# Performance work log

Hardware: AMD Instinct MI355X
Metric: run time of the kernel (lower is better)

## Reference

```python
import jax, jax.numpy as jnp
import numpy as np


def setup_inputs() -> dict:
    key = jax.random.key(0)
    k1, k2, k3, k4 = jax.random.split(key, 4)
    S, D, DKQ, DV = 8192, 2048, 128, 128
    x = jax.random.normal(k1, (S, D), dtype=jnp.float32)
    w_q = jax.random.uniform(k2, (D, DKQ), dtype=jnp.float32)
    w_k = jax.random.uniform(k3, (D, DKQ), dtype=jnp.float32)
    w_v = jax.random.uniform(k4, (D, DV), dtype=jnp.float32)
    return {"x": x, "w_q": w_q, "w_k": w_k, "w_v": w_v}


def reference(x, w_q, w_k, w_v):
    # x: [S, D]; single-head causal attention, unbatched as in the source.
    dim_kq = w_q.shape[1]
    q = x @ w_q  # [S, DKQ]
    k = x @ w_k  # [S, DKQ]
    v = x @ w_v  # [S, DV]
    scores = (q @ k.T) / jnp.sqrt(jnp.asarray(dim_kq, q.dtype))  # [S, S]
    S = scores.shape[0]
    causal = jnp.tril(jnp.ones((S, S), dtype=bool))
    scores = jnp.where(causal, scores, -jnp.inf)
    att_w = jax.nn.softmax(scores, axis=-1)
    return att_w @ v  # [S, DV]
```

## Files before the change

### kernel.cpp

```cpp
#include <hip/hip_runtime.h>

#define S_LEN 8192
#define D_DIM 2048
#define HD    128
#define KVB   32
#define NCH   16
#define QTR   256

typedef __attribute__((ext_vector_type(8))) short bf16x8;
typedef __attribute__((ext_vector_type(4))) float f32x4;

__device__ __forceinline__ unsigned short f2bf(float f) {
  unsigned int u = __float_as_uint(f);
  u += 0x7fffu + ((u >> 16) & 1u);
  return (unsigned short)(u >> 16);
}
__device__ __forceinline__ float bf2f(unsigned short h) {
  return __uint_as_float(((unsigned int)h) << 16);
}

__device__ __forceinline__ void glds16(const void* g, const short* l) {
  __builtin_amdgcn_global_load_lds(
      (const __attribute__((address_space(1))) void*)g,
      (__attribute__((address_space(3))) void*)l, 16, 0, 0);
}

__global__ __launch_bounds__(256)
void split_w_kernel(const float* __restrict__ wq, const float* __restrict__ wk,
                    const float* __restrict__ wv,
                    unsigned short* __restrict__ wTh, unsigned short* __restrict__ wTl)
{
  const int mode = blockIdx.y;
  const float* __restrict__ w = (mode == 0) ? wq : (mode == 1) ? wk : wv;
  unsigned short* __restrict__ oh = wTh + (size_t)mode * HD * D_DIM;
  unsigned short* __restrict__ ol = wTl + (size_t)mode * HD * D_DIM;
  const int k0 = blockIdx.x * 64;

  __shared__ float ws[64][132];
  const int t = threadIdx.x;
#pragma unroll
  for (int i = 0; i < 8; ++i) {
    int idx = t + i * 256;
    int row = idx >> 5;
    int c4  = idx & 31;
    *(float4*)&ws[row][c4 * 4] = *(const float4*)(w + (size_t)(k0 + row) * HD + c4 * 4);
  }
  __syncthreads();
#pragma unroll
  for (int i = 0; i < 4; ++i) {
    int task = t + i * 256;
    int col = task >> 3;
    int kc  = task & 7;
    ushort4 h[2], l[2];
#pragma unroll
    for (int e = 0; e < 8; ++e) {
      float f = ws[kc * 8 + e][col];
      unsigned short hb = f2bf(f);
      ((unsigned short*)&h[e >> 2])[e & 3] = hb;
      ((unsigned short*)&l[e >> 2])[e & 3] = f2bf(f - bf2f(hb));
    }
    size_t off = (size_t)col * D_DIM + k0 + kc * 8;
    *(ushort4*)(oh + off)     = h[0];
    *(ushort4*)(oh + off + 4) = h[1];
    *(ushort4*)(ol + off)     = l[0];
    *(ushort4*)(ol + off + 4) = l[1];
  }
}

__global__ __launch_bounds__(256)
void proj_kernel(const float* __restrict__ x,
                 const unsigned short* __restrict__ wTh, const unsigned short* __restrict__ wTl,
                 unsigned short* __restrict__ q_hi, unsigned short* __restrict__ q_lo,
                 unsigned short* __restrict__ k_hi, unsigned short* __restrict__ k_lo,
                 unsigned short* __restrict__ vT)
{
  __shared__ short sm[2][12288];

  const int mode = blockIdx.y;
  const int mt   = blockIdx.x;
  const bool split = (mode < 2);

  const unsigned short* gwh = wTh + (size_t)mode * HD * D_DIM;
  const unsigned short* gwl = wTl + (size_t)mode * HD * D_DIM;

  const int t   = threadIdx.x;
  const int wid = t >> 6;
  const int ln  = t & 63;
  const int cl  = ln & 15;
  const int g4  = ln >> 4;

  const int slotx = wid * 64 + ln;
  const int rowx  = slotx >> 2, scx = slotx & 3;
  const int kofx  = (scx ^ (rowx & 3)) * 8;
  const float* gx = x + (size_t)(mt * 64 + rowx) * D_DIM + kofx;

  auto stagew = [&](int kt, int buf) {
    short* b = sm[buf];
#pragma unroll
    for (int g = 0; g < 2; ++g) {
      int slot = g * 256 + wid * 64 + ln;
      int col = slot >> 2, sc = slot & 3;
      int kof = (sc ^ (col & 3)) * 8;
      glds16(gwh + (size_t)col * D_DIM + kt + kof, b + 4096 + (g * 256 + wid * 64) * 8);
      if (split)
        glds16(gwl + (size_t)col * D_DIM + kt + kof, b + 8192 + (g * 256 + wid * 64) * 8);
    }
  };
  auto writex = [&](const float4& a0, const float4& a1, int buf) {
    short* b = sm[buf];
    float fv[8];
    *(float4*)&fv[0] = a0;
    *(float4*)&fv[4] = a1;
    bf16x8 hv, lv;
#pragma unroll
    for (int e = 0; e < 8; ++e) {
      unsigned short hb = f2bf(fv[e]);
      hv[e] = (short)hb;
      lv[e] = (short)f2bf(fv[e] - bf2f(hb));
    }
    *(bf16x8*)(b + slotx * 8) = hv;
    if (split) *(bf16x8*)(b + 2048 + slotx * 8) = lv;
  };

  f32x4 acc[2][4];
#pragma unroll
  for (int m = 0; m < 2; ++m)
#pragma unroll
    for (int n = 0; n < 4; ++n) acc[m][n] = f32x4{0.f, 0.f, 0.f, 0.f};

  {
    float4 a0 = *(const float4*)(gx + 0);
    float4 a1 = *(const float4*)(gx + 4);
    stagew(0, 0);
    writex(a0, a1, 0);
  }
  __syncthreads();

  for (int kt = 0, step = 0; kt < D_DIM; kt += 32, ++step) {
    const int cur = step & 1;
    const bool more = (kt + 32 < D_DIM);
    float4 n0, n1;
    if (more) {
      n0 = *(const float4*)(gx + kt + 32);
      n1 = *(const float4*)(gx + kt + 36);
      stagew(kt + 32, cur ^ 1);
    }

    const short* b = sm[cur];
    bf16x8 a_h[2], a_l[2], b_h[4], b_l[4];
#pragma unroll
    for (int m = 0; m < 2; ++m) {
      int row = (wid >> 1) * 32 + m * 16 + cl;
      int byte = row * 64 + ((g4 ^ (row & 3)) << 4);
      a_h[m] = *(const bf16x8*)((const char*)b + byte);
      if (split) a_l[m] = *(const bf16x8*)((const char*)b + 4096 + byte);
    }
#pragma unroll
    for (int n = 0; n < 4; ++n) {
      int col = (wid & 1) * 64 + n * 16 + cl;
      int byte = col * 64 + ((g4 ^ (col & 3)) << 4);
      b_h[n] = *(const bf16x8*)((const char*)b + 8192 + byte);
      if (split) b_l[n] = *(const bf16x8*)((const char*)b + 16384 + byte);
    }

#pragma unroll
    for (int m = 0; m < 2; ++m)
#pragma unroll
      for (int n = 0; n < 4; ++n)
        acc[m][n] = __builtin_amdgcn_mfma_f32_16x16x32_bf16(a_h[m], b_h[n], acc[m][n], 0, 0, 0);
    if (split) {
#pragma unroll
      for (int m = 0; m < 2; ++m)
#pragma unroll
        for (int n = 0; n < 4; ++n) {
          acc[m][n] = __builtin_amdgcn_mfma_f32_16x16x32_bf16(a_l[m], b_h[n], acc[m][n], 0, 0, 0);
          acc[m][n] = __builtin_amdgcn_mfma_f32_16x16x32_bf16(a_h[m], b_l[n], acc[m][n], 0, 0, 0);
        }
    }
    if (more) writex(n0, n1, cur ^ 1);
    __syncthreads();
  }

  const int rbase = mt * 64 + (wid >> 1) * 32 + g4 * 4;
  const int cbase = (wid & 1) * 64 + cl;

  if (mode < 2) {
    const float scale = (mode == 0) ? 0.08838834764831843f : 1.0f;
    unsigned short* __restrict__ oh = (mode == 0) ? q_hi : k_hi;
    unsigned short* __restrict__ ol = (mode == 0) ? q_lo : k_lo;
#pragma unroll
    for (int m = 0; m < 2; ++m)
#pragma unroll
      for (int n = 0; n < 4; ++n)
#pragma unroll
        for (int r = 0; r < 4; ++r) {
          float val = acc[m][n][r] * scale;
          unsigned short hb = f2bf(val);
          size_t off = (size_t)(rbase + m * 16 + r) * HD + cbase + n * 16;
          oh[off] = hb;
          ol[off] = f2bf(val - bf2f(hb));
        }
  } else {
#pragma unroll
    for (int m = 0; m < 2; ++m)
#pragma unroll
      for (int n = 0; n < 4; ++n) {
        ushort4 o;
#pragma unroll
        for (int r = 0; r < 4; ++r) ((unsigned short*)&o)[r] = f2bf(acc[m][n][r]);
        int col = cbase + n * 16;
        *(ushort4*)(vT + (size_t)col * S_LEN + rbase + m * 16) = o;
      }
  }
}

__global__ __launch_bounds__(512)
void attn_kernel(const unsigned short* __restrict__ q_hi, const unsigned short* __restrict__ q_lo,
                 const unsigned short* __restrict__ k_hi, const unsigned short* __restrict__ k_lo,
                 const unsigned short* __restrict__ vT,
                 unsigned short* __restrict__ part_o, float* __restrict__ part_ml)
{
  extern __shared__ short smem[];
  short* ls_kh = smem;
  short* ls_kl = ls_kh + 8192;
  short* ls_v  = ls_kl + 8192;
  short* ls_ql = ls_v + 8192;
  short* ls_p  = ls_ql + 32768;

  const int t   = threadIdx.x;
  const int wid = t >> 6;
  const int ln  = t & 63;
  const int cl  = ln & 15;
  const int g4  = ln >> 4;
  const int pairId = blockIdx.x >> 4;
  const int chunk  = blockIdx.x & 15;

  short* pw = ls_p + wid * 1280;

  auto stage = [&](int j, int buf) {
    const unsigned short* gkh = k_hi + (size_t)j * KVB * HD;
    const unsigned short* gkl = k_lo + (size_t)j * KVB * HD;
    const unsigned short* gv  = vT + (size_t)j * KVB;
    {
      int row = t >> 4, sc = t & 15;
      int c16 = sc ^ (row & 7);
      glds16(gkh + row * HD + c16 * 8, ls_kh + buf * 4096 + t * 8);
      glds16(gkl + row * HD + c16 * 8, ls_kl + buf * 4096 + t * 8);
    }
    {
      int d = t >> 2, sub = t & 3;
      int s2 = sub ^ ((d >> 1) & 3);
      glds16(gv + (size_t)d * S_LEN + s2 * 8, ls_v + buf * 4096 + t * 8);
    }
  };

  for (int hh = 0; hh < 2; ++hh) {
    const int T = hh ? (31 - pairId) : pairId;
    const int jmaxB = 8 * T + 7;
    const int jmaxW = 8 * T + wid;
    const int rowbase = T * QTR + wid * 32;

    {
      const unsigned short* gql = q_lo + (size_t)T * QTR * HD;
#pragma unroll
      for (int i = 0; i < 8; ++i) {
        int slot = i * 512 + t;
        int row = slot >> 4, sc = slot & 15;
        int c16 = sc ^ (row & 7);
        glds16(gql + (size_t)row * HD + c16 * 8, ls_ql + slot * 8);
      }
    }

    bf16x8 qh[2][4];
#pragma unroll
    for (int rg = 0; rg < 2; ++rg) {
      const size_t qoff = ((size_t)rowbase + rg * 16 + cl) * HD + g4 * 8;
#pragma unroll
      for (int kc = 0; kc < 4; ++kc)
        qh[rg][kc] = *(const bf16x8*)(q_hi + qoff + kc * 32);
    }

    float m_i[2][4], l_i[2][4];
    f32x4 o_acc[2][8];
#pragma unroll
    for (int rg = 0; rg < 2; ++rg)
#pragma unroll
      for (int i = 0; i < 4; ++i) { m_i[rg][i] = -1e30f; l_i[rg][i] = 0.f; }
#pragma unroll
    for (int rg = 0; rg < 2; ++rg)
#pragma unroll
      for (int c2 = 0; c2 < 8; ++c2) o_acc[rg][c2] = f32x4{0.f, 0.f, 0.f, 0.f};

    if (chunk <= jmaxB) {
      int cur = 0;
      stage(chunk, 0);
      __syncthreads();
      for (int j = chunk; j <= jmaxB; j += NCH) {
        if (j + NCH <= jmaxB) stage(j + NCH, cur ^ 1);

        if (j <= jmaxW) {
          const int rl0 = wid * 32 + cl;
          const int rl1 = rl0 + 16;
          f32x4 s[2][2];
          s[0][0] = f32x4{0.f, 0.f, 0.f, 0.f};
          s[0][1] = f32x4{0.f, 0.f, 0.f, 0.f};
          s[1][0] = f32x4{0.f, 0.f, 0.f, 0.f};
          s[1][1] = f32x4{0.f, 0.f, 0.f, 0.f};
          __builtin_amdgcn_s_setprio(1);
#pragma unroll
          for (int kc = 0; kc < 4; ++kc) {
            const int ch = kc * 4 + g4;
            bf16x8 ql0 = *(const bf16x8*)((const char*)ls_ql + rl0 * 256 + ((ch ^ (rl0 & 7)) << 4));
            bf16x8 ql1 = *(const bf16x8*)((const char*)ls_ql + rl1 * 256 + ((ch ^ (rl1 & 7)) << 4));
#pragma unroll
            for (int c = 0; c < 2; ++c) {
              const int kcol = c * 16 + cl;
              const int byteK = kcol * 256 + ((ch ^ (kcol & 7)) << 4);
              bf16x8 khf = *(const bf16x8*)((const char*)(ls_kh + cur * 4096) + byteK);
              bf16x8 klf = *(const bf16x8*)((const char*)(ls_kl + cur * 4096) + byteK);
              s[0][c] = __builtin_amdgcn_mfma_f32_16x16x32_bf16(qh[0][kc], khf, s[0][c], 0, 0, 0);
              s[0][c] = __builtin_amdgcn_mfma_f32_16x16x32_bf16(ql0,      khf, s[0][c], 0, 0, 0);
              s[0][c] = __builtin_amdgcn_mfma_f32_16x16x32_bf16(qh[0][kc], klf, s[0][c], 0, 0, 0);
              s[1][c] = __builtin_amdgcn_mfma_f32_16x16x32_bf16(qh[1][kc], khf, s[1][c], 0, 0, 0);
              s[1][c] = __builtin_amdgcn_mfma_f32_16x16x32_bf16(ql1,      khf, s[1][c], 0, 0, 0);
              s[1][c] = __builtin_amdgcn_mfma_f32_16x16x32_bf16(qh[1][kc], klf, s[1][c], 0, 0, 0);
            }
          }
          __builtin_amdgcn_s_setprio(0);

          if (j == jmaxW) {
#pragma unroll
            for (int rg = 0; rg < 2; ++rg)
#pragma unroll
              for (int c = 0; c < 2; ++c)
#pragma unroll
                for (int i = 0; i < 4; ++i) {
                  int col = j * KVB + c * 16 + cl;
                  int row = rowbase + rg * 16 + g4 * 4 + i;
                  if (col > row) s[rg][c][i] = -1e30f;
                }
          }

          bool ok = true;
#pragma unroll
          for (int rg = 0; rg < 2; ++rg)
#pragma unroll
            for (int i = 0; i < 4; ++i) {
              float mx = fmaxf(s[rg][0][i], s[rg][1][i]);
              ok = ok && (mx <= m_i[rg][i] + 8.0f);
            }
          if (!__all(ok)) {
#pragma unroll
            for (int rg = 0; rg < 2; ++rg)
#pragma unroll
              for (int i = 0; i < 4; ++i) {
                float rm = fmaxf(s[rg][0][i], s[rg][1][i]);
                rm = fmaxf(rm, __shfl_xor(rm, 1));
                rm = fmaxf(rm, __shfl_xor(rm, 2));
                rm = fmaxf(rm, __shfl_xor(rm, 4));
                rm = fmaxf(rm, __shfl_xor(rm, 8));
                float mnew = fmaxf(m_i[rg][i], rm);
                float corr = __expf(m_i[rg][i] - mnew);
                l_i[rg][i] *= corr;
#pragma unroll
                for (int c2 = 0; c2 < 8; ++c2) o_acc[rg][c2][i] *= corr;
                m_i[rg][i] = mnew;
              }
          }

#pragma unroll
          for (int rg = 0; rg < 2; ++rg)
#pragma unroll
            for (int c = 0; c < 2; ++c)
#pragma unroll
              for (int i = 0; i < 4; ++i) {
                float sv = s[rg][c][i];
                float p = (sv > -1e29f) ? __expf(sv - m_i[rg][i]) : 0.f;
                l_i[rg][i] += p;
                pw[(rg * 16 + g4 * 4 + i) * 40 + c * 16 + cl] = (short)f2bf(p);
              }

          bf16x8 pa0 = *(const bf16x8*)((const char*)pw + cl * 80 + g4 * 16);
          bf16x8 pa1 = *(const bf16x8*)((const char*)pw + (16 + cl) * 80 + g4 * 16);
          __builtin_amdgcn_s_setprio(1);
#pragma unroll
          for (int c2 = 0; c2 < 8; ++c2) {
            const int d0 = c2 * 16 + cl;
            const int byteV = d0 * 64 + ((g4 ^ ((d0 >> 1) & 3)) << 4);
            bf16x8 vb = *(const bf16x8*)((const char*)(ls_v + cur * 4096) + byteV);
            o_acc[0][c2] = __builtin_amdgcn_mfma_f32_16x16x32_bf16(pa0, vb, o_acc[0][c2], 0, 0, 0);
            o_acc[1][c2] = __builtin_amdgcn_mfma_f32_16x16x32_bf16(pa1, vb, o_acc[1][c2], 0, 0, 0);
          }
          __builtin_amdgcn_s_setprio(0);
        }

        __syncthreads();
        cur ^= 1;
      }
    }

    const int base = T * NCH + chunk;
#pragma unroll
    for (int rg = 0; rg < 2; ++rg)
#pragma unroll
      for (int c2 = 0; c2 < 8; ++c2)
#pragma unroll
        for (int i = 0; i < 4; ++i) {
          int row = wid * 32 + rg * 16 + g4 * 4 + i;
          part_o[((size_t)base * QTR + row) * HD + c2 * 16 + cl] = f2bf(o_acc[rg][c2][i]);
        }

#pragma unroll
    for (int rg = 0; rg < 2; ++rg)
#pragma unroll
      for (int i = 0; i < 4; ++i) {
        float lv = l_i[rg][i];
        lv += __shfl_xor(lv, 1);
        lv += __shfl_xor(lv, 2);
        lv += __shfl_xor(lv, 4);
        lv += __shfl_xor(lv, 8);
        if (cl == 0) {
          int row = wid * 32 + rg * 16 + g4 * 4 + i;
          part_ml[base * 512 + row]       = m_i[rg][i];
          part_ml[base * 512 + 256 + row] = lv;
        }
      }
  }
}

__global__ __launch_bounds__(128)
void merge_kernel(const unsigned short* __restrict__ part_o, const float* __restrict__ part_ml,
                  float* __restrict__ out)
{
  const int row = blockIdx.x;
  const int T   = row >> 8;
  const int r   = row & 255;
  const int c   = threadIdx.x;

  float m[NCH], l[NCH];
  float mstar = -3e38f;
#pragma unroll
  for (int s = 0; s < NCH; ++s) {
    m[s] = part_ml[(T * NCH + s) * 512 + r];
    l[s] = part_ml[(T * NCH + s) * 512 + 256 + r];
    mstar = fmaxf(mstar, m[s]);
  }
  float num = 0.f, den = 0.f;
#pragma unroll
  for (int s = 0; s < NCH; ++s) {
    float wgt = __expf(m[s] - mstar);
    den += l[s] * wgt;
    num += wgt * bf2f(part_o[((size_t)(T * NCH + s) * QTR + r) * HD + c]);
  }
  out[(size_t)row * HD + c] = num / den;
}

extern "C" void kernel_launch(void* const* d_in, const int* in_sizes, int n_in,
                              void* d_out, int out_size, void* d_ws, size_t ws_size,
                              hipStream_t stream)
{
  const float* x  = (const float*)d_in[0];
  const float* wq = (const float*)d_in[1];
  const float* wk = (const float*)d_in[2];
  const float* wv = (const float*)d_in[3];
  float* out = (float*)d_out;

  unsigned short* p = (unsigned short*)d_ws;
  unsigned short* xh = p;  p += (size_t)S_LEN * D_DIM;
  unsigned short* xl = p;  p += (size_t)S_LEN * D_DIM;
  unsigned short* wTh = p; p += (size_t)3 * HD * D_DIM;
  unsigned short* wTl = p; p += (size_t)3 * HD * D_DIM;
  unsigned short* q_hi = p; p += (size_t)S_LEN * HD;
  unsigned short* q_lo = p; p += (size_t)S_LEN * HD;
  unsigned short* k_hi = p; p += (size_t)S_LEN * HD;
  unsigned short* k_lo = p; p += (size_t)S_LEN * HD;
  unsigned short* vT   = p; p += (size_t)S_LEN * HD;
  unsigned short* part_o = xh;
  float* part_ml = (float*)wTh;

  split_w_kernel<<<dim3(32, 3), 256, 0, stream>>>(wq, wk, wv, wTh, wTl);
  proj_kernel<<<dim3(128, 3), 256, 0, stream>>>(x, wTh, wTl,
                                                q_hi, q_lo, k_hi, k_lo, vT);
  const int smem_bytes = (8192 * 3 + 32768 + 8 * 1280) * (int)sizeof(short);
  attn_kernel<<<dim3(256), 512, smem_bytes, stream>>>(q_hi, q_lo, k_hi, k_lo, vT,
                                                      part_o, part_ml);
  merge_kernel<<<dim3(8192), 128, 0, stream>>>(part_o, part_ml, out);
}
```

Baseline: 137.4 us.

## Split projection GEMM along K and add reduction kernel

The projection kernel is split into two halves along the D dimension, going from 384 blocks to 768 blocks, to improve occupancy across the GPU's compute units. Each half writes fp32 partial sums to a workspace. A new reduce kernel adds the two halves, applies the scale and hi/lo bf16 split, and transposes V through shared memory for coalesced writes. This costs an extra kernel launch and extra global traffic for the fp32 partials, about 24 MB written and then read back.

```diff
diff --git a/kernel.cpp b/kernel.cpp
--- a/kernel.cpp
+++ b/kernel.cpp
@@ -68,20 +68,20 @@
 }
 
 __global__ __launch_bounds__(256)
-void proj_kernel(const float* __restrict__ x,
-                 const unsigned short* __restrict__ wTh, const unsigned short* __restrict__ wTl,
-                 unsigned short* __restrict__ q_hi, unsigned short* __restrict__ q_lo,
-                 unsigned short* __restrict__ k_hi, unsigned short* __restrict__ k_lo,
-                 unsigned short* __restrict__ vT)
+void proj_sk_kernel(const float* __restrict__ x,
+                    const unsigned short* __restrict__ wTh, const unsigned short* __restrict__ wTl,
+                    float* __restrict__ pp)
 {
   __shared__ short sm[2][12288];
 
   const int mode = blockIdx.y;
   const int mt   = blockIdx.x;
+  const int kz   = blockIdx.z;
   const bool split = (mode < 2);
-
-  const unsigned short* gwh = wTh + (size_t)mode * HD * D_DIM;
-  const unsigned short* gwl = wTl + (size_t)mode * HD * D_DIM;
+  const int kbase = kz * (D_DIM / 2);
+
+  const unsigned short* gwh = wTh + (size_t)mode * HD * D_DIM + kbase;
+  const unsigned short* gwl = wTl + (size_t)mode * HD * D_DIM + kbase;
 
   const int t   = threadIdx.x;
   const int wid = t >> 6;
@@ -92,7 +92,7 @@
   const int slotx = wid * 64 + ln;
   const int rowx  = slotx >> 2, scx = slotx & 3;
   const int kofx  = (scx ^ (rowx & 3)) * 8;
-  const float* gx = x + (size_t)(mt * 64 + rowx) * D_DIM + kofx;
+  const float* gx = x + (size_t)(mt * 64 + rowx) * D_DIM + kbase + kofx;
 
   auto stagew = [&](int kt, int buf) {
     short* b = sm[buf];
@@ -136,9 +136,10 @@
   }
   __syncthreads();
 
-  for (int kt = 0, step = 0; kt < D_DIM; kt += 32, ++step) {
+  const int KHALF = D_DIM / 2;
+  for (int kt = 0, step = 0; kt < KHALF; kt += 32, ++step) {
     const int cur = step & 1;
-    const bool more = (kt + 32 < D_DIM);
+    const bool more = (kt + 32 < KHALF);
     float4 n0, n1;
     if (more) {
       n0 = *(const float4*)(gx + kt + 32);
@@ -183,34 +184,73 @@
 
   const int rbase = mt * 64 + (wid >> 1) * 32 + g4 * 4;
   const int cbase = (wid & 1) * 64 + cl;
+  float* op = pp + ((size_t)(mode * 2 + kz)) * S_LEN * HD;
+#pragma unroll
+  for (int m = 0; m < 2; ++m)
+#pragma unroll
+    for (int n = 0; n < 4; ++n)
+#pragma unroll
+      for (int r = 0; r < 4; ++r)
+        op[(size_t)(rbase + m * 16 + r) * HD + cbase + n * 16] = acc[m][n][r];
+}
+
+__global__ __launch_bounds__(256)
+void reduce_split_kernel(const float* __restrict__ pp,
+                         unsigned short* __restrict__ q_hi, unsigned short* __restrict__ q_lo,
+                         unsigned short* __restrict__ k_hi, unsigned short* __restrict__ k_lo,
+                         unsigned short* __restrict__ vT)
+{
+  __shared__ float tile[64][132];
+  const int mode = blockIdx.y;
+  const int mt   = blockIdx.x;
+  const int t    = threadIdx.x;
+
+  const float* p0 = pp + ((size_t)(mode * 2 + 0)) * S_LEN * HD + (size_t)mt * 64 * HD;
+  const float* p1 = pp + ((size_t)(mode * 2 + 1)) * S_LEN * HD + (size_t)mt * 64 * HD;
 
   if (mode < 2) {
     const float scale = (mode == 0) ? 0.08838834764831843f : 1.0f;
     unsigned short* __restrict__ oh = (mode == 0) ? q_hi : k_hi;
     unsigned short* __restrict__ ol = (mode == 0) ? q_lo : k_lo;
 #pragma unroll
-    for (int m = 0; m < 2; ++m)
-#pragma unroll
-      for (int n = 0; n < 4; ++n)
-#pragma unroll
-        for (int r = 0; r < 4; ++r) {
-          float val = acc[m][n][r] * scale;
-          unsigned short hb = f2bf(val);
-          size_t off = (size_t)(rbase + m * 16 + r) * HD + cbase + n * 16;
-          oh[off] = hb;
-          ol[off] = f2bf(val - bf2f(hb));
-        }
+    for (int i = 0; i < 8; ++i) {
+      int off = i * 1024 + t * 4;
+      float4 a = *(const float4*)(p0 + off);
+      float4 b = *(const float4*)(p1 + off);
+      ushort4 hv, lv;
+#pragma unroll
+      for (int e = 0; e < 4; ++e) {
+        float s = (((const float*)&a)[e] + ((const float*)&b)[e]) * scale;
+        unsigned short hb = f2bf(s);
+        ((unsigned short*)&hv)[e] = hb;
+        ((unsigned short*)&lv)[e] = f2bf(s - bf2f(hb));
+      }
+      int row = off >> 7, col = off & 127;
+      size_t go = (size_t)(mt * 64 + row) * HD + col;
+      *(ushort4*)(oh + go) = hv;
+      *(ushort4*)(ol + go) = lv;
+    }
   } else {
 #pragma unroll
-    for (int m = 0; m < 2; ++m)
-#pragma unroll
-      for (int n = 0; n < 4; ++n) {
-        ushort4 o;
-#pragma unroll
-        for (int r = 0; r < 4; ++r) ((unsigned short*)&o)[r] = f2bf(acc[m][n][r]);
-        int col = cbase + n * 16;
-        *(ushort4*)(vT + (size_t)col * S_LEN + rbase + m * 16) = o;
-      }
+    for (int i = 0; i < 8; ++i) {
+      int off = i * 1024 + t * 4;
+      float4 a = *(const float4*)(p0 + off);
+      float4 b = *(const float4*)(p1 + off);
+      int row = off >> 7, col = off & 127;
+      float4 s;
+      s.x = a.x + b.x; s.y = a.y + b.y; s.z = a.z + b.z; s.w = a.w + b.w;
+      *(float4*)&tile[row][col] = s;
+    }
+    __syncthreads();
+    const int col = t >> 1, half = t & 1;
+#pragma unroll
+    for (int r8 = 0; r8 < 4; ++r8) {
+      bf16x8 v;
+#pragma unroll
+      for (int e = 0; e < 8; ++e)
+        v[e] = (short)f2bf(tile[half * 32 + r8 * 8 + e][col]);
+      *(bf16x8*)(vT + (size_t)col * S_LEN + mt * 64 + half * 32 + r8 * 8) = v;
+    }
   }
 }
 
@@ -476,11 +516,12 @@
   unsigned short* k_lo = p; p += (size_t)S_LEN * HD;
   unsigned short* vT   = p; p += (size_t)S_LEN * HD;
   unsigned short* part_o = xh;
+  float* pp = (float*)xl;
   float* part_ml = (float*)wTh;
 
   split_w_kernel<<<dim3(32, 3), 256, 0, stream>>>(wq, wk, wv, wTh, wTl);
-  proj_kernel<<<dim3(128, 3), 256, 0, stream>>>(x, wTh, wTl,
-                                                q_hi, q_lo, k_hi, k_lo, vT);
+  proj_sk_kernel<<<dim3(128, 3, 2), 256, 0, stream>>>(x, wTh, wTl, pp);
+  reduce_split_kernel<<<dim3(128, 3), 256, 0, stream>>>(pp, q_hi, q_lo, k_hi, k_lo, vT);
   const int smem_bytes = (8192 * 3 + 32768 + 8 * 1280) * (int)sizeof(short);
   attn_kernel<<<dim3(256), 512, smem_bytes, stream>>>(q_hi, q_lo, k_hi, k_lo, vT,
                                                       part_o, part_ml);
```

Result: faster. 129.5 us, median of 2 (-5.7%).
